# Optimization experiments

Measured on AMD Instinct MI355X. Metric: run time of the kernel, lower is better.

## Reference

```python
import jax, jax.numpy as jnp
import numpy as np

S = 2_000_000   # sequence length (tokens/residues)
P = 1_000_000   # number of 'positive' (pu) indices
E = 20          # number of experts / alphabet size


def setup_inputs() -> dict:
    key = jax.random.key(0)
    k1, k2, k3, k4, k5 = jax.random.split(key, 5)
    # x[0, :, :20] acts as per-token one-hot over the 20-letter alphabet;
    # argmax of uniform noise gives a valid routing index per token.
    x = jax.random.uniform(k1, (1, S, E), dtype=jnp.float32)
    h = jax.random.normal(k2, (S, 2), dtype=jnp.float32)        # 'output1' from inner model
    W = jax.random.normal(k3, (E, 2, 2), dtype=jnp.float32) * 0.5  # per-expert Linear weight [out,in]
    b = jax.random.normal(k4, (E, 2), dtype=jnp.float32) * 0.1     # per-expert Linear bias
    # unique, sorted positive indices (torch.index_select semantics)
    pu_index = jnp.sort(jax.random.permutation(k5, S)[:P]).astype(jnp.int32)
    return {"x": x, "h": h, "W": W, "b": b, "pu_index": pu_index}


def reference(x, h, W, b, pu_index):
    # recognize_res: per-token expert index from one-hot channels 0:20 of x[0]
    res_index = jnp.argmax(x[0, :, :E], axis=-1)                 # [S] int
    # verblizer_function: per-token expert Linear(2,2) + Softmax, fused as
    # gather expert params -> batched matmul -> softmax
    Wt = W[res_index]                                            # [S, 2, 2]
    bt = b[res_index]                                            # [S, 2]
    y = jnp.einsum('si,soi->so', h, Wt) + bt                     # torch Linear: h @ W.T + b
    y = jax.nn.softmax(y, axis=-1)                               # output1 after verblizer
    # pu_train: rows at pu_index first (in pu order), remaining rows after
    n_tok = h.shape[0]
    mask = jnp.zeros((n_tok,), dtype=bool).at[pu_index].set(True)
    non = jnp.nonzero(~mask, size=n_tok - pu_index.shape[0])[0]  # preserves original order
    perm = jnp.concatenate([pu_index.astype(non.dtype), non])
    y2 = y[perm]                                                 # output2
    return (y, y2)
```

## Files before the change

kernel.cpp:

```cpp
#include <hip/hip_runtime.h>
#include <math.h>

__global__ __launch_bounds__(256) void verblizer_fused_kernel(
    const float* __restrict__ x,
    const float* __restrict__ h,
    const float* __restrict__ W,
    const float* __restrict__ b,
    const int*   __restrict__ pu,
    float*       __restrict__ out,
    int S, int P)
{
    __shared__ float sW[80];
    __shared__ float sb[40];
    int tid = threadIdx.x;
    if (tid < 80)  sW[tid] = W[tid];
    else if (tid < 120) sb[tid - 80] = b[tid - 80];
    __syncthreads();

    int s = blockIdx.x * blockDim.x + tid;
    if (s >= S) return;

    const float4* xv = (const float4*)(x + (size_t)s * 20);
    float best = -INFINITY;
    int   bi   = 0;
#pragma unroll
    for (int j = 0; j < 5; ++j) {
        float4 v = xv[j];
        if (v.x > best) { best = v.x; bi = j * 4 + 0; }
        if (v.y > best) { best = v.y; bi = j * 4 + 1; }
        if (v.z > best) { best = v.z; bi = j * 4 + 2; }
        if (v.w > best) { best = v.w; bi = j * 4 + 3; }
    }

    float2 hv = ((const float2*)h)[s];
    const float* we = sW + bi * 4;
    float y0 = fmaf(hv.x, we[0], fmaf(hv.y, we[1], sb[bi * 2 + 0]));
    float y1 = fmaf(hv.x, we[2], fmaf(hv.y, we[3], sb[bi * 2 + 1]));

    float m  = fmaxf(y0, y1);
    float e0 = __expf(y0 - m);
    float e1 = __expf(y1 - m);
    float inv = 1.0f / (e0 + e1);
    float2 yo = make_float2(e0 * inv, e1 * inv);

    ((float2*)out)[s] = yo;

    int lo = 0, hi = P;
    while (lo < hi) {
        int mid = (lo + hi) >> 1;
        if (pu[mid] < s) lo = mid + 1; else hi = mid;
    }
    int dst = (lo < P && pu[lo] == s) ? lo : (P + s - lo);
    ((float2*)(out + (size_t)2 * S))[dst] = yo;
}

extern "C" void kernel_launch(void* const* d_in, const int* in_sizes, int n_in,
                              void* d_out, int out_size, void* d_ws, size_t ws_size,
                              hipStream_t stream) {
    const float* x  = (const float*)d_in[0];
    const float* h  = (const float*)d_in[1];
    const float* W  = (const float*)d_in[2];
    const float* b  = (const float*)d_in[3];
    const int*   pu = (const int*)d_in[4];

    const int S = in_sizes[1] / 2;
    const int P = in_sizes[4];

    float* out = (float*)d_out;

    const int block = 256;
    const int grid  = (S + block - 1) / block;
    verblizer_fused_kernel<<<grid, block, 0, stream>>>(x, h, W, b, pu, out, S, P);
}
```

Baseline: 262.7 us.

## Coalesce x loads via shared staging and replace per-thread binary search with block ballot ranks

Threads now load the block's x rows as contiguous float4 chunks, take a partial argmax per chunk, and stage the results in shared memory, so global reads of x are coalesced instead of each thread striding 80 bytes. The per-thread binary search over pu is replaced by two searches per block that bound the pu range, followed by flag marking and a wave ballot/popcount prefix to compute each token's destination rank. This removes about 20 dependent global loads per thread but adds shared memory use and extra barriers. Ties in the argmax still resolve to the first index because chunks are scanned in order with a strict comparison.

```diff
diff --git a/kernel.cpp b/kernel.cpp
--- a/kernel.cpp
+++ b/kernel.cpp
@@ -1,57 +1,104 @@
 #include <hip/hip_runtime.h>
 #include <math.h>
 
-__global__ __launch_bounds__(256) void verblizer_fused_kernel(
-    const float* __restrict__ x,
-    const float* __restrict__ h,
-    const float* __restrict__ W,
-    const float* __restrict__ b,
-    const int*   __restrict__ pu,
-    float*       __restrict__ out,
+#define TPB 256
+
+__global__ __launch_bounds__(TPB) void verblizer_fused_kernel(
+    const float4* __restrict__ x4,
+    const float2* __restrict__ h2,
+    const float*  __restrict__ W,
+    const float*  __restrict__ b,
+    const int*    __restrict__ pu,
+    float2*       __restrict__ y,
+    float2*       __restrict__ y2,
     int S, int P)
 {
     __shared__ float sW[80];
     __shared__ float sb[40];
-    int tid = threadIdx.x;
-    if (tid < 80)  sW[tid] = W[tid];
-    else if (tid < 120) sb[tid - 80] = b[tid - 80];
+    __shared__ uint2 pairs[TPB * 5];
+    __shared__ int   flags[TPB];
+    __shared__ int   r0s, r1s;
+    __shared__ int   wsum[TPB / 64];
+
+    const int t  = threadIdx.x;
+    const int B0 = blockIdx.x * TPB;
+    const int nb = min(TPB, S - B0);
+
+    if (t < 80)       sW[t]      = W[t];
+    else if (t < 120) sb[t - 80] = b[t - 80];
+    flags[t] = 0;
+
+    if (t < 2) {
+        int target = (t == 0) ? B0 : (B0 + nb);
+        int lo = 0, hi = P;
+        while (lo < hi) {
+            int mid = (lo + hi) >> 1;
+            if (pu[mid] < target) lo = mid + 1; else hi = mid;
+        }
+        if (t == 0) r0s = lo; else r1s = lo;
+    }
+
+    const int nchunk = nb * 5;
+    const float4* xb = x4 + (size_t)B0 * 5;
+#pragma unroll
+    for (int j = 0; j < 5; ++j) {
+        int m = t + TPB * j;
+        if (m < nchunk) {
+            float4 v  = xb[m];
+            int   tok = m / 5;
+            int   c   = m - 5 * tok;
+            float best = v.x; int bi = 0;
+            if (v.y > best) { best = v.y; bi = 1; }
+            if (v.z > best) { best = v.z; bi = 2; }
+            if (v.w > best) { best = v.w; bi = 3; }
+            pairs[tok * 5 + c] = make_uint2(__float_as_uint(best), (unsigned)(4 * c + bi));
+        }
+    }
     __syncthreads();
 
-    int s = blockIdx.x * blockDim.x + tid;
-    if (s >= S) return;
+    const int r0 = r0s;
+    const int nmark = r1s - r0;
+    if (t < nmark) flags[pu[r0 + t] - B0] = 1;
+    __syncthreads();
 
-    const float4* xv = (const float4*)(x + (size_t)s * 20);
-    float best = -INFINITY;
-    int   bi   = 0;
+    const bool f   = (t < nb) && flags[t];
+    const unsigned long long mask = __ballot(f);
+    const int lane = t & 63;
+    const int w    = t >> 6;
+    if (lane == 0) wsum[w] = __popcll(mask);
+    const int cnt = __popcll(mask & ((1ull << lane) - 1ull));
+    __syncthreads();
+
+    if (t >= nb) return;
+
+    int base = 0;
 #pragma unroll
-    for (int j = 0; j < 5; ++j) {
-        float4 v = xv[j];
-        if (v.x > best) { best = v.x; bi = j * 4 + 0; }
-        if (v.y > best) { best = v.y; bi = j * 4 + 1; }
-        if (v.z > best) { best = v.z; bi = j * 4 + 2; }
-        if (v.w > best) { best = v.w; bi = j * 4 + 3; }
+    for (int ww = 0; ww < TPB / 64; ++ww)
+        if (ww < w) base += wsum[ww];
+    const int s    = B0 + t;
+    const int rank = r0 + base + cnt;
+
+    float best = -INFINITY; int bi = 0;
+#pragma unroll
+    for (int c = 0; c < 5; ++c) {
+        uint2 p = pairs[t * 5 + c];
+        float v = __uint_as_float(p.x);
+        if (v > best) { best = v; bi = (int)p.y; }
     }
 
-    float2 hv = ((const float2*)h)[s];
+    float2 hv = h2[s];
     const float* we = sW + bi * 4;
     float y0 = fmaf(hv.x, we[0], fmaf(hv.y, we[1], sb[bi * 2 + 0]));
     float y1 = fmaf(hv.x, we[2], fmaf(hv.y, we[3], sb[bi * 2 + 1]));
-
-    float m  = fmaxf(y0, y1);
-    float e0 = __expf(y0 - m);
-    float e1 = __expf(y1 - m);
+    float mx = fmaxf(y0, y1);
+    float e0 = __expf(y0 - mx);
+    float e1 = __expf(y1 - mx);
     float inv = 1.0f / (e0 + e1);
     float2 yo = make_float2(e0 * inv, e1 * inv);
 
-    ((float2*)out)[s] = yo;
-
-    int lo = 0, hi = P;
-    while (lo < hi) {
-        int mid = (lo + hi) >> 1;
-        if (pu[mid] < s) lo = mid + 1; else hi = mid;
-    }
-    int dst = (lo < P && pu[lo] == s) ? lo : (P + s - lo);
-    ((float2*)(out + (size_t)2 * S))[dst] = yo;
+    y[s] = yo;
+    const int dst = f ? rank : (P + s - rank);
+    y2[dst] = yo;
 }
 
 extern "C" void kernel_launch(void* const* d_in, const int* in_sizes, int n_in,
@@ -66,9 +113,10 @@
     const int S = in_sizes[1] / 2;
     const int P = in_sizes[4];
 
-    float* out = (float*)d_out;
+    float2* y  = (float2*)d_out;
+    float2* y2 = (float2*)d_out + S;
 
-    const int block = 256;
-    const int grid  = (S + block - 1) / block;
-    verblizer_fused_kernel<<<grid, block, 0, stream>>>(x, h, W, b, pu, out, S, P);
+    const int grid = (S + TPB - 1) / TPB;
+    verblizer_fused_kernel<<<grid, TPB, 0, stream>>>(
+        (const float4*)x, (const float2*)h, W, b, pu, y, y2, S, P);
 }
```

New measurement: 274.6 us. 1.05x slower.
